# Performance work log

Measured on AMD Instinct MI355X. Metric: run time of the kernel, lower is better.

Reference implementation:

```python
import jax, jax.numpy as jnp
import numpy as np

NUM_HEADS = 16
HEAD_SIZE = 64
D_MODEL = NUM_HEADS * HEAD_SIZE  # 1024


def setup_inputs() -> dict:
    key = jax.random.key(0)
    ks = jax.random.split(key, 12)
    B, S = 4, 2048
    q = jax.random.normal(ks[0], (B, S, D_MODEL), dtype=jnp.float32)
    k = jax.random.normal(ks[1], (B, S, D_MODEL), dtype=jnp.float32)
    v = jax.random.normal(ks[2], (B, S, D_MODEL), dtype=jnp.float32)
    w = jax.random.uniform(ks[3], (B, S), dtype=jnp.float32)
    scale = 1.0 / np.sqrt(D_MODEL)
    Wq = jax.random.normal(ks[4], (D_MODEL, D_MODEL), dtype=jnp.float32) * scale
    Wk = jax.random.normal(ks[5], (D_MODEL, D_MODEL), dtype=jnp.float32) * scale
    Wv = jax.random.normal(ks[6], (D_MODEL, D_MODEL), dtype=jnp.float32) * scale
    Wo = jax.random.normal(ks[7], (D_MODEL, D_MODEL), dtype=jnp.float32) * scale
    bq = jnp.zeros((D_MODEL,), jnp.float32)
    bk = jnp.zeros((D_MODEL,), jnp.float32)
    bv = jnp.zeros((D_MODEL,), jnp.float32)
    bo = jnp.zeros((D_MODEL,), jnp.float32)
    return {"q": q, "k": k, "v": v, "w": w,
            "Wq": Wq, "bq": bq, "Wk": Wk, "bk": bk,
            "Wv": Wv, "bv": bv, "Wo": Wo, "bo": bo}


def reference(q, k, v, w, Wq, bq, Wk, bk, Wv, bv, Wo, bo):
    B, S, _ = q.shape
    H, Dh = NUM_HEADS, HEAD_SIZE

    def split_heads(x):  # [B,S,D] -> [B,H,S,Dh]
        return x.reshape(B, -1, H, Dh).transpose(0, 2, 1, 3)

    q_h = split_heads(q @ Wq + bq)
    k_h = split_heads(k @ Wk + bk)
    v_h = split_heads(v @ Wv + bv)

    # [B,H,Sq,Sk]
    score = jnp.einsum('bhqd,bhkd->bhqk', q_h, k_h) / jnp.sqrt(
        jnp.asarray(Dh, jnp.float32))
    # weighted unnormalized softmax: exp(score)*w / sum (no max subtraction,
    # faithful to original)
    exp_score = jnp.exp(score) * w[:, None, None, :]
    attn = exp_score / (jnp.sum(exp_score, axis=-1, keepdims=True) + 1e-12)

    context = jnp.einsum('bhqk,bhkd->bhqd', attn, v_h)  # [B,H,S,Dh]
    context = context.transpose(0, 2, 1, 3).reshape(B, -1, H * Dh)
    return context @ Wo + bo
```

## Files before the change

### kernel.cpp

```cpp
#include <hip/hip_runtime.h>
#include <hip/hip_bf16.h>

typedef __bf16 bf16x8 __attribute__((ext_vector_type(8)));
typedef float f32x4 __attribute__((ext_vector_type(4)));
typedef float f32x16 __attribute__((ext_vector_type(16)));
typedef unsigned short u16;
typedef unsigned int u32;

#define SB 4
#define SS 2048
#define SD 1024
#define SH 16
#define SDH 64

__device__ __forceinline__ u16 f2bf(float f) {
  u32 r;
  asm("v_cvt_pk_bf16_f32 %0, %1, %1" : "=v"(r) : "v"(f));
  return (u16)r;
}

__device__ __forceinline__ void gl_lds16(const void* g, void* l) {
  __builtin_amdgcn_global_load_lds(
      (__attribute__((address_space(1))) void*)g,
      (__attribute__((address_space(3))) void*)l, 16, 0, 0);
}

__global__ void prep_kernel(const float* __restrict__ q,
                            const float* __restrict__ k,
                            const float* __restrict__ v,
                            u32* __restrict__ oq, u32* __restrict__ ok,
                            u32* __restrict__ ov,
                            const float* __restrict__ w,
                            float* __restrict__ lwg,
                            const float* __restrict__ W0,
                            const float* __restrict__ W1,
                            const float* __restrict__ W2,
                            const float* __restrict__ W3,
                            u16* __restrict__ T0, u16* __restrict__ T1,
                            u16* __restrict__ T2, u16* __restrict__ T3) {
  __shared__ float t[32][33];
  int bid = blockIdx.x, tid = threadIdx.x;
  if (bid < 12288) {
    int sel = bid >> 12;
    int i = (bid & 4095) * 256 + tid;
    const float* in = (sel == 0) ? q : (sel == 1) ? k : v;
    u32* out = (sel == 0) ? oq : (sel == 1) ? ok : ov;
    const float4* inp = (const float4*)in;
    float4 a = inp[2 * i], b = inp[2 * i + 1];
    uint4 o;
    asm("v_cvt_pk_bf16_f32 %0, %1, %2" : "=v"(o.x) : "v"(a.x), "v"(a.y));
    asm("v_cvt_pk_bf16_f32 %0, %1, %2" : "=v"(o.y) : "v"(a.z), "v"(a.w));
    asm("v_cvt_pk_bf16_f32 %0, %1, %2" : "=v"(o.z) : "v"(b.x), "v"(b.y));
    asm("v_cvt_pk_bf16_f32 %0, %1, %2" : "=v"(o.w) : "v"(b.z), "v"(b.w));
    ((uint4*)out)[i] = o;
  } else if (bid < 16384) {
    int local = bid - 12288;
    int z = local >> 10, by = (local >> 5) & 31, bx = local & 31;
    const float* W = (z == 0) ? W0 : (z == 1) ? W1 : (z == 2) ? W2 : W3;
    u16* Wt = (z == 0) ? T0 : (z == 1) ? T1 : (z == 2) ? T2 : T3;
    int tx = tid & 31, ty = tid >> 5;
#pragma unroll
    for (int j = 0; j < 32; j += 8)
      t[ty + j][tx] = W[(size_t)(by * 32 + ty + j) * SD + bx * 32 + tx];
    __syncthreads();
#pragma unroll
    for (int j = 0; j < 32; j += 8)
      Wt[(size_t)(bx * 32 + ty + j) * SD + by * 32 + tx] = f2bf(t[tx][ty + j]);
  } else {
    int i = (bid - 16384) * 256 + tid;
    int b = i >> 11, kk = i & 2047;
    int pos = ((kk >> 5) << 5) | (((kk >> 2) & 1) << 4) |
              (((kk >> 3) & 3) << 2) | (kk & 3);
    lwg[(b << 11) + pos] = __builtin_amdgcn_logf(w[i]);
  }
}

template <int MODE>
__global__ __launch_bounds__(256, 2)
void gemm_bt(const u16* __restrict__ A, const u16* __restrict__ Bt,
             const float* __restrict__ bias, void* __restrict__ Out,
             int M, int N, int K) {
  __shared__ u16 Asl[2][128 * 64];
  __shared__ u16 Bsl[2][128 * 64];
  const int ntile = N >> 7;
  int bid = blockIdx.x;
  bid = (bid & 7) * ((int)gridDim.x >> 3) + (bid >> 3);
  int m0 = (bid / ntile) * 128, n0 = (bid % ntile) * 128;
  int tid = threadIdx.x;
  int lane = tid & 63, wv = tid >> 6;
  int wr = wv >> 1, wc = wv & 1;

  auto stage = [&](int buf, int k0) {
#pragma unroll
    for (int it = 0; it < 4; ++it) {
      int c = tid + it * 256;
      int row = c >> 3, sl = c & 7;
      int ssl = sl ^ (row & 7);
      gl_lds16(A + (size_t)(m0 + row) * K + k0 + ssl * 8,
               (char*)&Asl[buf][0] + c * 16);
      gl_lds16(Bt + (size_t)(n0 + row) * K + k0 + ssl * 8,
               (char*)&Bsl[buf][0] + c * 16);
    }
  };

  f32x4 acc[4][4] = {};
  stage(0, 0);

  int nk = K >> 6;
  for (int kt = 0; kt < nk; ++kt) {
    int buf = kt & 1;
    if (kt + 1 < nk) {
      stage(buf ^ 1, (kt + 1) << 6);
      asm volatile("s_waitcnt vmcnt(8) lgkmcnt(0)" ::: "memory");
    } else {
      asm volatile("s_waitcnt vmcnt(0) lgkmcnt(0)" ::: "memory");
    }
    __builtin_amdgcn_s_barrier();
#pragma unroll
    for (int kk = 0; kk < 2; ++kk) {
      bf16x8 af[4], bfr[4];
#pragma unroll
      for (int i = 0; i < 4; ++i) {
        int ar = wr * 64 + i * 16 + (lane & 15);
        int abyt = (ar * 128 + (kk * 32 + (lane >> 4) * 8) * 2) ^
                   ((ar & 7) << 4);
        af[i] = *(const bf16x8*)((const char*)&Asl[buf][0] + abyt);
        int br = wc * 64 + i * 16 + (lane & 15);
        int bbyt = (br * 128 + (kk * 32 + (lane >> 4) * 8) * 2) ^
                   ((br & 7) << 4);
        bfr[i] = *(const bf16x8*)((const char*)&Bsl[buf][0] + bbyt);
      }
#pragma unroll
      for (int i = 0; i < 4; ++i)
#pragma unroll
        for (int j = 0; j < 4; ++j)
          acc[i][j] = __builtin_amdgcn_mfma_f32_16x16x32_bf16(
              af[i], bfr[j], acc[i][j], 0, 0, 0);
    }
    __builtin_amdgcn_s_barrier();
  }

  int cg = lane >> 4, cc = lane & 15;
#pragma unroll
  for (int i = 0; i < 4; ++i) {
#pragma unroll
    for (int j = 0; j < 4; ++j) {
#pragma unroll
      for (int r = 0; r < 4; ++r) {
        int m = m0 + wr * 64 + i * 16 + cg * 4 + r;
        int n = n0 + wc * 64 + j * 16 + cc;
        float val = acc[i][j][r];
        if (MODE == 0) {
          val = (val + bias[n]) * 0.18033688011112042f;
          int b = m >> 11, s2 = m & 2047, h = n >> 6, dh = n & 63;
          ((u16*)Out)[((size_t)((b * SH + h) * SS + s2) << 6) + dh] =
              f2bf(val);
        } else if (MODE == 1) {
          val += bias[n];
          int b = m >> 11, s2 = m & 2047, h = n >> 6, dh = n & 63;
          size_t off = ((size_t)(b * SH + h) << 17) +
                       ((size_t)(s2 >> 5) << 11) + ((size_t)(dh >> 4) << 9) +
                       ((size_t)((s2 & 31) | ((dh & 8) << 2)) << 3) +
                       (dh & 7);
          ((u16*)Out)[off] = f2bf(val);
        } else if (MODE == 2) {
          val += bias[m];
          int h = m >> 6, dh = m & 63, b = n >> 11, s2 = n & 2047;
          size_t off = ((size_t)(b * SH + h) << 17) +
                       ((size_t)(s2 >> 4) << 10) + ((size_t)(dh >> 5) << 9) +
                       ((size_t)(((s2 >> 3) & 1) * 32 + (dh & 31)) << 3) +
                       (s2 & 7);
          ((u16*)Out)[off] = f2bf(val);
        } else {
          val += bias[n];
          ((float*)Out)[(size_t)m * N + n] = val;
        }
      }
    }
  }
}

__global__ __launch_bounds__(256, 4)
void attn_kernel(const u16* __restrict__ Qh, const u16* __restrict__ Kf,
                 const u16* __restrict__ Vf, const float* __restrict__ lwg,
                 u16* __restrict__ Ctx) {
  __shared__ u16 Kl[2][4096];
  __shared__ u16 Vl[2][4096];
  __shared__ __align__(64) float lwl[SS];

  int bid = blockIdx.x;
  int swz = (bid & 7) * 128 + (bid >> 3);
  int bh = swz >> 4;
  int qt = swz & 15;
  int b = bh >> 4, hh = bh & 15;
  int q0 = qt * 128;
  int tid = threadIdx.x, lane = tid & 63, qw = tid >> 6;
  int ql = lane & 31, h = lane >> 5;
  const size_t basebh = (size_t)bh * (SS * SDH);
  const char* Ksrc = (const char*)(Kf + basebh);
  const char* Vsrc = (const char*)(Vf + basebh);

  {
    const float4* src = (const float4*)(lwg + b * SS);
    float4 r0 = src[tid];
    float4 r1 = src[tid + 256];
    ((float4*)lwl)[tid] = r0;
    ((float4*)lwl)[tid + 256] = r1;
  }

  bf16x8 qf[4];
  {
    const u16* qp = Qh + basebh + (size_t)(q0 + qw * 32 + ql) * SDH + h * 8;
#pragma unroll
    for (int st = 0; st < 4; ++st) qf[st] = *(const bf16x8*)(qp + st * 16);
  }

  auto stageK = [&](int s, int t) {
    const char* p = Ksrc + (size_t)t * 8192;
    gl_lds16(p + tid * 16, (char*)&Kl[s][0] + tid * 16);
    gl_lds16(p + 4096 + tid * 16, (char*)&Kl[s][0] + 4096 + tid * 16);
  };
  auto stageV = [&](int s, int t) {
    const char* p = Vsrc + (size_t)t * 8192;
    gl_lds16(p + tid * 16, (char*)&Vl[s][0] + tid * 16);
    gl_lds16(p + 4096 + tid * 16, (char*)&Vl[s][0] + 4096 + tid * 16);
  };

  f32x16 ctx0 = {}, ctx1 = {};
  float rs = 0.f;
  u32 pk[8][2];

  auto qk = [&](int t) {
    const char* Ks = (const char*)&Kl[t & 1][0];
#pragma unroll
    for (int kt = 0; kt < 2; ++kt) {
      bf16x8 kf[4];
#pragma unroll
      for (int st = 0; st < 4; ++st)
        kf[st] = *(const bf16x8*)(Ks + (kt * 4 + st) * 1024 + lane * 16);
      f32x16 sc = *(const f32x16*)(lwl + (t * 2 + kt) * 32 + h * 16);
      __builtin_amdgcn_s_setprio(1);
#pragma unroll
      for (int st = 0; st < 4; ++st)
        sc = __builtin_amdgcn_mfma_f32_32x32x16_bf16(kf[st], qf[st], sc,
                                                     0, 0, 0);
      __builtin_amdgcn_s_setprio(0);
#pragma unroll
      for (int e2 = 0; e2 < 4; ++e2) {
        float v0 = __builtin_amdgcn_exp2f(sc[e2 * 4 + 0]);
        float v1 = __builtin_amdgcn_exp2f(sc[e2 * 4 + 1]);
        float v2 = __builtin_amdgcn_exp2f(sc[e2 * 4 + 2]);
        float v3 = __builtin_amdgcn_exp2f(sc[e2 * 4 + 3]);
        rs += (v0 + v1) + (v2 + v3);
        u32 p0, p1;
        asm("v_cvt_pk_bf16_f32 %0, %1, %2" : "=v"(p0) : "v"(v0), "v"(v1));
        asm("v_cvt_pk_bf16_f32 %0, %1, %2" : "=v"(p1) : "v"(v2), "v"(v3));
        pk[kt * 4 + e2][0] = p0;
        pk[kt * 4 + e2][1] = p1;
      }
    }
  };

  auto pv = [&](int t) {
    const char* Vs = (const char*)&Vl[t & 1][0];
#pragma unroll
    for (int ksl = 0; ksl < 4; ++ksl) {
      bf16x8 vf0 = *(const bf16x8*)(Vs + (ksl * 2 + 0) * 1024 + lane * 16);
      bf16x8 vf1 = *(const bf16x8*)(Vs + (ksl * 2 + 1) * 1024 + lane * 16);
      u32 d0 = pk[2 * ksl][0], d1 = pk[2 * ksl][1];
      u32 s0 = pk[2 * ksl + 1][0], s1 = pk[2 * ksl + 1][1];
      asm("v_permlane32_swap_b32 %0, %1" : "+v"(d0), "+v"(s0));
      asm("v_permlane32_swap_b32 %0, %1" : "+v"(d1), "+v"(s1));
      union { u32 uu[4]; bf16x8 v; } pa;
      pa.uu[0] = d0; pa.uu[1] = d1; pa.uu[2] = s0; pa.uu[3] = s1;
      __builtin_amdgcn_s_setprio(1);
      ctx0 = __builtin_amdgcn_mfma_f32_32x32x16_bf16(pa.v, vf0, ctx0, 0, 0, 0);
      ctx1 = __builtin_amdgcn_mfma_f32_32x32x16_bf16(pa.v, vf1, ctx1, 0, 0, 0);
      __builtin_amdgcn_s_setprio(0);
    }
  };

  stageK(0, 0);
  stageV(0, 0);
  asm volatile("s_waitcnt lgkmcnt(0)" ::: "memory");
  __builtin_amdgcn_s_barrier();

  for (int t = 0; t < 31; ++t) {
    asm volatile("s_waitcnt vmcnt(2)" ::: "memory");
    __builtin_amdgcn_s_barrier();
    stageK((t + 1) & 1, t + 1);
    stageV((t + 1) & 1, t + 1);
    qk(t);
    asm volatile("s_waitcnt vmcnt(4)" ::: "memory");
    pv(t);
  }
  asm volatile("s_waitcnt vmcnt(2)" ::: "memory");
  __builtin_amdgcn_s_barrier();
  qk(31);
  asm volatile("s_waitcnt vmcnt(0)" ::: "memory");
  pv(31);

  rs += __shfl_xor(rs, 32, 64);
  float rinv = 1.0f / (rs + 1e-12f);
#pragma unroll
  for (int reg = 0; reg < 16; ++reg) {
    int qrow = (reg & 3) + 8 * (reg >> 2) + 4 * h;
    float ri = __shfl(rinv, qrow, 64);
    int srow = q0 + qw * 32 + qrow;
    size_t base = ((size_t)(b * SS + srow) << 10) + hh * SDH;
    Ctx[base + ql] = f2bf(ctx0[reg] * ri);
    Ctx[base + 32 + ql] = f2bf(ctx1[reg] * ri);
  }
}

extern "C" void kernel_launch(void* const* d_in, const int* in_sizes, int n_in,
                              void* d_out, int out_size, void* d_ws,
                              size_t ws_size, hipStream_t stream) {
  const float* q = (const float*)d_in[0];
  const float* k = (const float*)d_in[1];
  const float* v = (const float*)d_in[2];
  const float* w = (const float*)d_in[3];
  const float* Wq = (const float*)d_in[4];
  const float* bq = (const float*)d_in[5];
  const float* Wk = (const float*)d_in[6];
  const float* bk = (const float*)d_in[7];
  const float* Wv = (const float*)d_in[8];
  const float* bv = (const float*)d_in[9];
  const float* Wo = (const float*)d_in[10];
  const float* bo = (const float*)d_in[11];
  float* out = (float*)d_out;

  char* ws = (char*)d_ws;
  const size_t SZ = (size_t)8192 * 1024 * 2;
  u16* qb = (u16*)(ws);
  u16* kb = (u16*)(ws + SZ);
  u16* vb = (u16*)(ws + 2 * SZ);
  u16* WqT = (u16*)(ws + 3 * SZ);
  u16* WkT = WqT + 1024 * 1024;
  u16* WvT = WkT + 1024 * 1024;
  u16* WoT = WvT + 1024 * 1024;
  u16* Qh = (u16*)(ws + 3 * SZ + (size_t)4 * 1024 * 1024 * 2);
  u16* Kf = Qh + (size_t)8192 * 1024;
  u16* Vf = Kf + (size_t)8192 * 1024;
  float* lwg = (float*)(ws + 3 * SZ + (size_t)4 * 1024 * 1024 * 2 +
                        (size_t)3 * 8192 * 1024 * 2);
  u16* Ctx = qb;

  prep_kernel<<<16416, 256, 0, stream>>>(q, k, v, (u32*)qb, (u32*)kb,
                                         (u32*)vb, w, lwg, Wq, Wk, Wv, Wo,
                                         WqT, WkT, WvT, WoT);

  gemm_bt<0><<<512, 256, 0, stream>>>(qb, WqT, bq, Qh, 8192, 1024, 1024);
  gemm_bt<1><<<512, 256, 0, stream>>>(kb, WkT, bk, Kf, 8192, 1024, 1024);
  gemm_bt<2><<<512, 256, 0, stream>>>(WvT, vb, bv, Vf, 1024, 8192, 1024);

  attn_kernel<<<1024, 256, 0, stream>>>(Qh, Kf, Vf, lwg, Ctx);

  gemm_bt<3><<<512, 256, 0, stream>>>(Ctx, WoT, bo, out, 8192, 1024, 1024);
}
```

Measured before the change: 210.6 us.

## Give each wave private K/V LDS buffers and drop block barriers in attention loop

The attention kernel now stages K and V tiles per wave into private double-buffered LDS regions, with 32-key tiles instead of 64, so waves no longer need a workgroup barrier each iteration. Synchronisation uses only per-wave vmcnt waits. This removes barrier stalls and lets waves drift independently. In exchange each wave loads the same K/V data separately, quadrupling global/L2 traffic into LDS. LDS usage roughly doubles, and launch bounds drop to 2 blocks per SIMD, which lowers occupancy.

After: 238.5 us. 1.13x slower.

```diff
diff --git a/kernel.cpp b/kernel.cpp
--- a/kernel.cpp
+++ b/kernel.cpp
@@ -180,12 +180,12 @@
   }
 }
 
-__global__ __launch_bounds__(256, 4)
+__global__ __launch_bounds__(256, 2)
 void attn_kernel(const u16* __restrict__ Qh, const u16* __restrict__ Kf,
                  const u16* __restrict__ Vf, const float* __restrict__ lwg,
                  u16* __restrict__ Ctx) {
-  __shared__ u16 Kl[2][4096];
-  __shared__ u16 Vl[2][4096];
+  __shared__ u16 Kl[4][2][2048];
+  __shared__ u16 Vl[4][2][2048];
   __shared__ __align__(64) float lwl[SS];
 
   int bid = blockIdx.x;
@@ -216,55 +216,55 @@
   }
 
   auto stageK = [&](int s, int t) {
-    const char* p = Ksrc + (size_t)t * 8192;
-    gl_lds16(p + tid * 16, (char*)&Kl[s][0] + tid * 16);
-    gl_lds16(p + 4096 + tid * 16, (char*)&Kl[s][0] + 4096 + tid * 16);
+    const char* p = Ksrc + (size_t)t * 4096;
+    char* d = (char*)&Kl[qw][s][0];
+#pragma unroll
+    for (int it = 0; it < 4; ++it)
+      gl_lds16(p + (lane + it * 64) * 16, d + (lane + it * 64) * 16);
   };
   auto stageV = [&](int s, int t) {
-    const char* p = Vsrc + (size_t)t * 8192;
-    gl_lds16(p + tid * 16, (char*)&Vl[s][0] + tid * 16);
-    gl_lds16(p + 4096 + tid * 16, (char*)&Vl[s][0] + 4096 + tid * 16);
+    const char* p = Vsrc + (size_t)t * 4096;
+    char* d = (char*)&Vl[qw][s][0];
+#pragma unroll
+    for (int it = 0; it < 4; ++it)
+      gl_lds16(p + (lane + it * 64) * 16, d + (lane + it * 64) * 16);
   };
 
   f32x16 ctx0 = {}, ctx1 = {};
   float rs = 0.f;
-  u32 pk[8][2];
+  u32 pk[4][2];
 
   auto qk = [&](int t) {
-    const char* Ks = (const char*)&Kl[t & 1][0];
-#pragma unroll
-    for (int kt = 0; kt < 2; ++kt) {
-      bf16x8 kf[4];
-#pragma unroll
-      for (int st = 0; st < 4; ++st)
-        kf[st] = *(const bf16x8*)(Ks + (kt * 4 + st) * 1024 + lane * 16);
-      f32x16 sc = *(const f32x16*)(lwl + (t * 2 + kt) * 32 + h * 16);
-      __builtin_amdgcn_s_setprio(1);
-#pragma unroll
-      for (int st = 0; st < 4; ++st)
-        sc = __builtin_amdgcn_mfma_f32_32x32x16_bf16(kf[st], qf[st], sc,
-                                                     0, 0, 0);
-      __builtin_amdgcn_s_setprio(0);
-#pragma unroll
-      for (int e2 = 0; e2 < 4; ++e2) {
-        float v0 = __builtin_amdgcn_exp2f(sc[e2 * 4 + 0]);
-        float v1 = __builtin_amdgcn_exp2f(sc[e2 * 4 + 1]);
-        float v2 = __builtin_amdgcn_exp2f(sc[e2 * 4 + 2]);
-        float v3 = __builtin_amdgcn_exp2f(sc[e2 * 4 + 3]);
-        rs += (v0 + v1) + (v2 + v3);
-        u32 p0, p1;
-        asm("v_cvt_pk_bf16_f32 %0, %1, %2" : "=v"(p0) : "v"(v0), "v"(v1));
-        asm("v_cvt_pk_bf16_f32 %0, %1, %2" : "=v"(p1) : "v"(v2), "v"(v3));
-        pk[kt * 4 + e2][0] = p0;
-        pk[kt * 4 + e2][1] = p1;
-      }
+    const char* Ks = (const char*)&Kl[qw][t & 1][0];
+    bf16x8 kf[4];
+#pragma unroll
+    for (int st = 0; st < 4; ++st)
+      kf[st] = *(const bf16x8*)(Ks + st * 1024 + lane * 16);
+    f32x16 sc = *(const f32x16*)(lwl + t * 32 + h * 16);
+    __builtin_amdgcn_s_setprio(1);
+#pragma unroll
+    for (int st = 0; st < 4; ++st)
+      sc = __builtin_amdgcn_mfma_f32_32x32x16_bf16(kf[st], qf[st], sc,
+                                                   0, 0, 0);
+    __builtin_amdgcn_s_setprio(0);
+#pragma unroll
+    for (int e2 = 0; e2 < 4; ++e2) {
+      float v0 = __builtin_amdgcn_exp2f(sc[e2 * 4 + 0]);
+      float v1 = __builtin_amdgcn_exp2f(sc[e2 * 4 + 1]);
+      float v2 = __builtin_amdgcn_exp2f(sc[e2 * 4 + 2]);
+      float v3 = __builtin_amdgcn_exp2f(sc[e2 * 4 + 3]);
+      rs += (v0 + v1) + (v2 + v3);
+      asm("v_cvt_pk_bf16_f32 %0, %1, %2"
+          : "=v"(pk[e2][0]) : "v"(v0), "v"(v1));
+      asm("v_cvt_pk_bf16_f32 %0, %1, %2"
+          : "=v"(pk[e2][1]) : "v"(v2), "v"(v3));
     }
   };
 
   auto pv = [&](int t) {
-    const char* Vs = (const char*)&Vl[t & 1][0];
-#pragma unroll
-    for (int ksl = 0; ksl < 4; ++ksl) {
+    const char* Vs = (const char*)&Vl[qw][t & 1][0];
+#pragma unroll
+    for (int ksl = 0; ksl < 2; ++ksl) {
       bf16x8 vf0 = *(const bf16x8*)(Vs + (ksl * 2 + 0) * 1024 + lane * 16);
       bf16x8 vf1 = *(const bf16x8*)(Vs + (ksl * 2 + 1) * 1024 + lane * 16);
       u32 d0 = pk[2 * ksl][0], d1 = pk[2 * ksl][1];
@@ -285,20 +285,16 @@
   asm volatile("s_waitcnt lgkmcnt(0)" ::: "memory");
   __builtin_amdgcn_s_barrier();
 
-  for (int t = 0; t < 31; ++t) {
-    asm volatile("s_waitcnt vmcnt(2)" ::: "memory");
-    __builtin_amdgcn_s_barrier();
+  for (int t = 0; t < 63; ++t) {
     stageK((t + 1) & 1, t + 1);
     stageV((t + 1) & 1, t + 1);
+    asm volatile("s_waitcnt vmcnt(8)" ::: "memory");
     qk(t);
-    asm volatile("s_waitcnt vmcnt(4)" ::: "memory");
     pv(t);
   }
-  asm volatile("s_waitcnt vmcnt(2)" ::: "memory");
-  __builtin_amdgcn_s_barrier();
-  qk(31);
   asm volatile("s_waitcnt vmcnt(0)" ::: "memory");
-  pv(31);
+  qk(63);
+  pv(63);
 
   rs += __shfl_xor(rs, 32, 64);
   float rinv = 1.0f / (rs + 1e-12f);
```
